# Optimization experiments

Measured on AMD Instinct MI355X. Metric: run time of the kernel, lower is better.

The kernel has to match this reference:

```python
import jax, jax.numpy as jnp
import numpy as np

B, F, D = 4096, 39, 16          # batch, num_field, embedding_size
V = 1000000                     # num_feat (vocab)
H1, H2 = 128, 128               # cin_layer_sizes
INPUT_DIM = F * D               # 624
FC_DIM = H1 // 2 + H2           # 192 (split_half)
DEEP = [400, 400]
BN_EPS = 1e-5


def setup_inputs() -> dict:
    key = jax.random.key(0)
    ks = jax.random.split(key, 16)
    xav = lambda k, shp: jax.random.normal(k, shp, jnp.float32) * np.sqrt(2.0 / (shp[0] + shp[-1]))
    return {
        "feat_index": jax.random.randint(ks[0], (B, F), 0, V),
        "feat_value": jax.random.uniform(ks[1], (B, F), jnp.float32),
        "emb_table": xav(ks[2], (V, D)),
        "linear_w": xav(ks[3], (INPUT_DIM, 1)),
        "linear_b": jnp.zeros((1,), jnp.float32),
        "conv_w1": xav(ks[4], (H1, F, F)),          # (out, h_prev, m) == conv1d 1x1 weight reshaped
        "conv_b1": jnp.zeros((H1,), jnp.float32),
        "conv_w2": xav(ks[5], (H2, H1 // 2, F)),
        "conv_b2": jnp.zeros((H2,), jnp.float32),
        "deep_w1": xav(ks[6], (INPUT_DIM, DEEP[0])),
        "deep_b1": jnp.zeros((DEEP[0],), jnp.float32),
        "bn_g1": jnp.ones((DEEP[0],), jnp.float32),
        "bn_b1": jnp.zeros((DEEP[0],), jnp.float32),
        "deep_w2": xav(ks[7], (DEEP[0], DEEP[1])),
        "deep_b2": jnp.zeros((DEEP[1],), jnp.float32),
        "bn_g2": jnp.ones((DEEP[1],), jnp.float32),
        "bn_b2": jnpp if False else jnp.zeros((DEEP[1],), jnp.float32),
        "out_w": xav(ks[8], (1 + FC_DIM + DEEP[1], 1)),
        "out_b": jnp.zeros((1,), jnp.float32),
    }


def _bn(x, g, b):
    # torch BatchNorm1d in training mode: biased batch variance
    m = x.mean(axis=0)
    v = x.var(axis=0)
    return g * (x - m) * jax.lax.rsqrt(v + BN_EPS) + b


def reference(feat_index, feat_value, emb_table, linear_w, linear_b,
              conv_w1, conv_b1, conv_w2, conv_b2,
              deep_w1, deep_b1, bn_g1, bn_b1,
              deep_w2, deep_b2, bn_g2, bn_b2,
              out_w, out_b):
    e = emb_table[feat_index]                      # [B, F, D]
    flat = e.reshape(e.shape[0], -1)               # [B, F*D]
    linear_part = flat @ linear_w + linear_b       # [B, 1]

    # CIN: fused outer-product + 1x1 conv (x_k[b,o,d] = sum_{h,m} W[o,h,m] x_prev[b,h,d] x0[b,m,d])
    x0 = e
    h1 = jax.nn.relu(jnp.einsum('bhd,bmd,ohm->bod', x0, x0, conv_w1) + conv_b1[None, :, None])
    nxt, hi1 = jnp.split(h1, 2, axis=1)            # split_half
    h2 = jax.nn.relu(jnp.einsum('bhd,bmd,ohm->bod', nxt, x0, conv_w2) + conv_b2[None, :, None])
    res = jnp.concatenate([hi1, h2], axis=1).sum(axis=2)   # [B, FC_DIM]

    # Deep tower (dropout off / deterministic)
    y = jax.nn.relu(_bn(flat @ deep_w1 + deep_b1, bn_g1, bn_b1))
    y = jax.nn.relu(_bn(y @ deep_w2 + deep_b2, bn_g2, bn_b2))

    cat = jnp.concatenate([linear_part, res, y], axis=1)   # [B, 593]
    return cat @ out_w + out_b
```

## Files before the change

kernel.cpp:

```cpp
#include <hip/hip_runtime.h>

#define BATCH   4096
#define NF      39
#define ED      16
#define IN_DIM  624
#define DW      400
#define BN_EPS  1e-5f
#define AK1     640
#define NKS1    20
#define NKS2    13
#define WCOL    416
#define NK1     117
#define NK2     156

typedef __attribute__((ext_vector_type(8))) short short8;
typedef __attribute__((ext_vector_type(16))) float f32x16;
typedef __attribute__((ext_vector_type(4))) float f32x4;
typedef __attribute__((ext_vector_type(2))) float f32x2;
typedef unsigned short u16;

__device__ inline unsigned pack_hi2(float a, float b) {
  return __builtin_amdgcn_perm(__float_as_uint(b), __float_as_uint(a), 0x07060302u);
}
__device__ inline unsigned bf16_rne(float f) {
  unsigned u = __float_as_uint(f);
  u += 0x7fff + ((u >> 16) & 1);
  return u >> 16;
}
__device__ inline float bf2f(u16 v) { return __uint_as_float((unsigned)v << 16); }

#define CIN1_E (NK1 * 2048)
#define CIN2_E (NK2 * 2048)
#define D1_E  (NKS1 * WCOL * 32)
#define D2_E  (NKS2 * WCOL * 32)
#define PREP_E (CIN1_E + CIN2_E + D1_E + D2_E + 1600)
#define PREP_B ((PREP_E + 255) / 256)
#define GATH_B (BATCH / 4)

__global__ __launch_bounds__(256) void k_gp(const int* __restrict__ idx,
    const float* __restrict__ emb, const float* __restrict__ lw,
    const float* __restrict__ lb, const float* __restrict__ w1,
    const float* __restrict__ w2, const float* __restrict__ dw1,
    const float* __restrict__ dw2, u16* __restrict__ flatb,
    float* __restrict__ lp, u16* __restrict__ wp1, u16* __restrict__ wp2,
    u16* __restrict__ wpd1, u16* __restrict__ wpd2, float* __restrict__ gstat) {
  int t = threadIdx.x;
  if (blockIdx.x < GATH_B) {
    int lane = t & 63;
    int b = blockIdx.x * 4 + (t >> 6);
    int sj = (lane < NF) ? idx[b * NF + lane] : 0;
    float acc = 0.f;
#pragma unroll
    for (int i = 0; i < 10; i++) {
      int e = lane + i * 64;
      if (e < IN_DIM) {
        int f = e >> 4;
        int row = __shfl(sj, f);
        float v = emb[(size_t)row * ED + (e & 15)];
        flatb[(size_t)b * AK1 + e] = (u16)bf16_rne(v);
        acc = fmaf(v, lw[e], acc);
      } else {
        flatb[(size_t)b * AK1 + e] = 0;
      }
    }
#pragma unroll
    for (int k = 1; k < 64; k <<= 1) acc += __shfl_xor(acc, k);
    if (lane == 0) lp[b] = acc + lb[0];
  } else {
    int e = (blockIdx.x - GATH_B) * 256 + t;
    if (e < CIN1_E) {
      int k16 = e >> 11, r = e & 2047, col = r >> 4, kk = r & 15;
      int mg = k16 / 3, sg = k16 - mg * 3;
      int h = sg * 16 + kk;
      wp1[e] = (h < NF) ? (u16)bf16_rne(w1[(size_t)col * (NF * NF) + h * NF + mg])
                        : (u16)0;
    } else if (e < CIN1_E + CIN2_E) {
      int e2 = e - CIN1_E;
      int k16 = e2 >> 11, r = e2 & 2047, col = r >> 4, kk = r & 15;
      int k = k16 * 16 + kk, h = k & 63, m = k >> 6;
      wp2[e2] = (u16)bf16_rne(w2[(size_t)col * (64 * NF) + h * NF + m]);
    } else if (e < CIN1_E + CIN2_E + D1_E) {
      int e2 = e - CIN1_E - CIN2_E;
      int ksg = e2 / (WCOL * 32), r = e2 - ksg * (WCOL * 32);
      int col = r >> 5, kk = r & 31;
      int k = ksg * 32 + kk;
      wpd1[e2] = (k < IN_DIM && col < DW) ? (u16)bf16_rne(dw1[(size_t)k * DW + col]) : 0;
    } else if (e < CIN1_E + CIN2_E + D1_E + D2_E) {
      int e2 = e - CIN1_E - CIN2_E - D1_E;
      int ksg = e2 / (WCOL * 32), r = e2 - ksg * (WCOL * 32);
      int col = r >> 5, kk = r & 31;
      int k = ksg * 32 + kk;
      wpd2[e2] = (k < DW && col < DW) ? (u16)bf16_rne(dw2[(size_t)k * DW + col]) : 0;
    } else if (e < PREP_E) {
      gstat[e - CIN1_E - CIN2_E - D1_E - D2_E] = 0.f;
    }
  }
}

__global__ __launch_bounds__(256, 2) void k_cin_f(
    const u16* __restrict__ flatb, const u16* __restrict__ wp1,
    const u16* __restrict__ wp2, const float* __restrict__ bias1,
    const float* __restrict__ bias2, float* __restrict__ res) {
  __shared__ __align__(16) u16 s1b[8 * 16 * 64];
  int t = threadIdx.x;
  int w = t >> 6, lane = t & 63;
  int sgrp = w & 1, oh = w >> 1;
  int col = lane & 31, khalf = lane >> 5;
  int si = (lane >> 4) & 1, d = lane & 15;
  int b0 = blockIdx.x * 8 + sgrp * 4;
  const u16* fb = flatb + (size_t)(b0 + si) * AK1;

  f32x2 sp1[2][3][4];
#pragma unroll
  for (int p = 0; p < 2; p++)
#pragma unroll
    for (int s = 0; s < 3; s++)
#pragma unroll
      for (int w4 = 0; w4 < 4; w4++) {
        int h0 = s * 16 + khalf * 8 + 2 * w4;
        int h1 = h0 + 1;
        float f0 = (h0 < NF) ? bf2f(fb[p * 1280 + h0 * 16 + d]) : 0.f;
        float f1 = (h1 < NF) ? bf2f(fb[p * 1280 + h1 * 16 + d]) : 0.f;
        sp1[p][s][w4] = (f32x2){f0, f1};
      }

  const u16* wb1 = wp1 + (size_t)(oh * 64 + col) * 16 + khalf * 8;
  short8 bfr[3][2];
#pragma unroll
  for (int k16 = 0; k16 < 2; k16++)
#pragma unroll
    for (int nt = 0; nt < 2; nt++)
      bfr[k16][nt] = *(const short8*)(wb1 + (size_t)k16 * 2048 + nt * 512);

  f32x16 acc[2][2];
#pragma unroll
  for (int p = 0; p < 2; p++)
#pragma unroll
    for (int nt = 0; nt < 2; nt++)
#pragma unroll
      for (int r = 0; r < 16; r++) acc[p][nt][r] = 0.f;

  float xv[2] = {bf2f(fb[d]), bf2f(fb[1280 + d])};
  float xvn[2];

#pragma unroll 1
  for (int mg = 0; mg < 13; mg++) {
#pragma unroll
    for (int j = 0; j < 9; j++) {
      int k16 = mg * 9 + j;
      int s = j % 3;
      if (s == 0) {
        int mn = mg * 3 + j / 3 + 1;
        xvn[0] = bf2f(fb[mn * 16 + d]);
        xvn[1] = bf2f(fb[1280 + mn * 16 + d]);
      }
      {
        const u16* wbp = wb1 + (size_t)(k16 + 2) * 2048;
#pragma unroll
        for (int nt = 0; nt < 2; nt++)
          bfr[(s + 2) % 3][nt] = *(const short8*)(wbp + nt * 512);
      }
      __builtin_amdgcn_s_setprio(1);
#pragma unroll
      for (int p = 0; p < 2; p++) {
        union { unsigned u[4]; short8 v; } a;
        f32x2 xv2 = (f32x2){xv[p], xv[p]};
#pragma unroll
        for (int w4 = 0; w4 < 4; w4++) {
          f32x2 pr = sp1[p][s][w4] * xv2;
          a.u[w4] = pack_hi2(pr[0], pr[1]);
        }
#pragma unroll
        for (int nt = 0; nt < 2; nt++)
          acc[p][nt] = __builtin_amdgcn_mfma_f32_32x32x16_bf16(
              a.v, bfr[s][nt], acc[p][nt], 0, 0, 0);
      }
      __builtin_amdgcn_s_setprio(0);
      if (s == 2) { xv[0] = xvn[0]; xv[1] = xvn[1]; }
    }
  }

  if (oh == 0) {
#pragma unroll
    for (int p = 0; p < 2; p++)
#pragma unroll
      for (int nt = 0; nt < 2; nt++) {
        int o = nt * 32 + col;
        float bi = bias1[o];
#pragma unroll
        for (int r = 0; r < 16; r++) {
          int smp = sgrp * 4 + p * 2 + (r >> 3);
          int dd = (r & 3) + 8 * ((r >> 2) & 1) + 4 * khalf;
          float v = fmaxf(acc[p][nt][r] + bi, 0.f);
          int ix = (((smp * 16 + dd) * 64) + o) ^ ((dd & 7) << 3);
          s1b[ix] = (u16)bf16_rne(v);
        }
      }
  } else {
#pragma unroll
    for (int p = 0; p < 2; p++)
#pragma unroll
      for (int nt = 0; nt < 2; nt++) {
        int o = 64 + nt * 32 + col;
        float bi = bias1[o];
        float p0 = 0.f, p1 = 0.f;
#pragma unroll
        for (int r = 0; r < 8; r++)  p0 += fmaxf(acc[p][nt][r] + bi, 0.f);
#pragma unroll
        for (int r = 8; r < 16; r++) p1 += fmaxf(acc[p][nt][r] + bi, 0.f);
        p0 += __shfl_xor(p0, 32);
        p1 += __shfl_xor(p1, 32);
        if (khalf == 0) {
          res[(size_t)(b0 + p * 2) * 192 + (o - 64)] = p0;
          res[(size_t)(b0 + p * 2 + 1) * 192 + (o - 64)] = p1;
        }
      }
  }

  const u16* wb2 = wp2 + (size_t)(oh * 64 + col) * 16 + khalf * 8;
  short8 bq[4][2];
#pragma unroll
  for (int k16 = 0; k16 < 3; k16++)
#pragma unroll
    for (int nt = 0; nt < 2; nt++)
      bq[k16][nt] = *(const short8*)(wb2 + (size_t)k16 * 2048 + nt * 512);

  __syncthreads();

  f32x2 sp2[2][4][4];
#pragma unroll
  for (int p = 0; p < 2; p++) {
    int smp = sgrp * 4 + p * 2 + si;
#pragma unroll
    for (int s = 0; s < 4; s++) {
      int ix = ((smp * 16 + d) * 64 + s * 16 + khalf * 8) ^ ((d & 7) << 3);
      union { short8 v; u16 e[8]; } vv;
      vv.v = *(const short8*)(s1b + ix);
#pragma unroll
      for (int w4 = 0; w4 < 4; w4++)
        sp2[p][s][w4] = (f32x2){bf2f(vv.e[2 * w4]), bf2f(vv.e[2 * w4 + 1])};
    }
  }

#pragma unroll
  for (int p = 0; p < 2; p++)
#pragma unroll
    for (int nt = 0; nt < 2; nt++)
#pragma unroll
      for (int r = 0; r < 16; r++) acc[p][nt][r] = 0.f;

  xv[0] = bf2f(fb[d]);
  xv[1] = bf2f(fb[1280 + d]);

#pragma unroll 1
  for (int mg = 0; mg < 13; mg++) {
#pragma unroll
    for (int j = 0; j < 12; j++) {
      int k16 = mg * 12 + j;
      int s = j & 3;
      if (s == 0) {
        int mn = mg * 3 + (j >> 2) + 1;
        xvn[0] = bf2f(fb[mn * 16 + d]);
        xvn[1] = bf2f(fb[1280 + mn * 16 + d]);
      }
      {
        const u16* wbp = wb2 + (size_t)(k16 + 3) * 2048;
#pragma unroll
        for (int nt = 0; nt < 2; nt++)
          bq[(j + 3) & 3][nt] = *(const short8*)(wbp + nt * 512);
      }
      __builtin_amdgcn_s_setprio(1);
#pragma unroll
      for (int p = 0; p < 2; p++) {
        union { unsigned u[4]; short8 v; } a;
        f32x2 xv2 = (f32x2){xv[p], xv[p]};
#pragma unroll
        for (int w4 = 0; w4 < 4; w4++) {
          f32x2 pr = sp2[p][s][w4] * xv2;
          a.u[w4] = pack_hi2(pr[0], pr[1]);
        }
#pragma unroll
        for (int nt = 0; nt < 2; nt++)
          acc[p][nt] = __builtin_amdgcn_mfma_f32_32x32x16_bf16(
              a.v, bq[s][nt], acc[p][nt], 0, 0, 0);
      }
      __builtin_amdgcn_s_setprio(0);
      if (s == 3) { xv[0] = xvn[0]; xv[1] = xvn[1]; }
    }
  }

#pragma unroll
  for (int p = 0; p < 2; p++)
#pragma unroll
    for (int nt = 0; nt < 2; nt++) {
      int o = oh * 64 + nt * 32 + col;
      float bi = bias2[o];
      float p0 = 0.f, p1 = 0.f;
#pragma unroll
      for (int r = 0; r < 8; r++)  p0 += fmaxf(acc[p][nt][r] + bi, 0.f);
#pragma unroll
      for (int r = 8; r < 16; r++) p1 += fmaxf(acc[p][nt][r] + bi, 0.f);
      p0 += __shfl_xor(p0, 32);
      p1 += __shfl_xor(p1, 32);
      if (khalf == 0) {
        res[(size_t)(b0 + p * 2) * 192 + 64 + o] = p0;
        res[(size_t)(b0 + p * 2 + 1) * 192 + 64 + o] = p1;
      }
    }
}

template <bool BN_A, int NKS, int KREAL, int AK>
__global__ __launch_bounds__(256) void k_gemm_mfma(
    const u16* __restrict__ Abf, const float* __restrict__ Af32,
    const u16* __restrict__ wp, const float* __restrict__ bias,
    const float* __restrict__ gsIn, const float* __restrict__ gs2In,
    const float* __restrict__ bng, const float* __restrict__ bnb,
    float* __restrict__ C, float* __restrict__ gs, float* __restrict__ gs2) {
  __shared__ float lsS[NKS * 32], lsH[NKS * 32];
  __shared__ float lred[64];
  int t = threadIdx.x;
  if (BN_A) {
    for (int c = t; c < NKS * 32; c += 256) {
      float sc = 0.f, sh = 0.f;
      if (c < DW) {
        float m = gsIn[c] * (1.f / BATCH);
        float var = gs2In[c] * (1.f / BATCH) - m * m;
        sc = bng[c] * rsqrtf(var + BN_EPS);
        sh = bnb[c] - m * sc;
      }
      lsS[c] = sc; lsH[c] = sh;
    }
  }
  if (t < 64) lred[t] = 0.f;
  __syncthreads();

  int w = t >> 6, lane = t & 63;
  int nl = lane & 15, q = lane >> 4;
  int row = blockIdx.x * 64 + w * 16 + nl;
  int c0 = blockIdx.y * 32;
  f32x4 acc[2];
  acc[0] = (f32x4){0.f, 0.f, 0.f, 0.f};
  acc[1] = (f32x4){0.f, 0.f, 0.f, 0.f};

  short8 araw[2]; f32x4 fraw0[2], fraw1[2]; short8 braw[2][2];
  auto loadA_raw = [&](int ksg, int buf) {
    int kb = ksg * 32 + q * 8;
    if (!BN_A) {
      araw[buf] = *(const short8*)(Abf + (size_t)row * AK + kb);
    } else {
      if (kb + 8 <= KREAL) {
        fraw0[buf] = *(const f32x4*)(Af32 + (size_t)row * KREAL + kb);
        fraw1[buf] = *(const f32x4*)(Af32 + (size_t)row * KREAL + kb + 4);
      } else {
        fraw0[buf] = (f32x4){0.f,0.f,0.f,0.f};
        fraw1[buf] = (f32x4){0.f,0.f,0.f,0.f};
      }
    }
    const u16* wb = wp + (size_t)ksg * (WCOL * 32) + (size_t)(c0 + nl) * 32 + q * 8;
    braw[buf][0] = *(const short8*)wb;
    braw[buf][1] = *(const short8*)(wb + 16 * 32);
  };
  auto cookA = [&](int ksg, int buf) -> short8 {
    if (!BN_A) return araw[buf];
    int kb = ksg * 32 + q * 8;
    f32x4 s0 = *(const f32x4*)&lsS[kb], h0 = *(const f32x4*)&lsH[kb];
    f32x4 s1 = *(const f32x4*)&lsS[kb + 4], h1 = *(const f32x4*)&lsH[kb + 4];
    union { unsigned u[4]; short8 s; } a;
    float v0 = fmaxf(fmaf(fraw0[buf][0], s0[0], h0[0]), 0.f);
    float v1 = fmaxf(fmaf(fraw0[buf][1], s0[1], h0[1]), 0.f);
    float v2 = fmaxf(fmaf(fraw0[buf][2], s0[2], h0[2]), 0.f);
    float v3 = fmaxf(fmaf(fraw0[buf][3], s0[3], h0[3]), 0.f);
    float v4 = fmaxf(fmaf(fraw1[buf][0], s1[0], h1[0]), 0.f);
    float v5 = fmaxf(fmaf(fraw1[buf][1], s1[1], h1[1]), 0.f);
    float v6 = fmaxf(fmaf(fraw1[buf][2], s1[2], h1[2]), 0.f);
    float v7 = fmaxf(fmaf(fraw1[buf][3], s1[3], h1[3]), 0.f);
    a.u[0] = bf16_rne(v0) | (bf16_rne(v1) << 16);
    a.u[1] = bf16_rne(v2) | (bf16_rne(v3) << 16);
    a.u[2] = bf16_rne(v4) | (bf16_rne(v5) << 16);
    a.u[3] = bf16_rne(v6) | (bf16_rne(v7) << 16);
    return a.s;
  };

  loadA_raw(0, 0);
#pragma unroll 4
  for (int ksg = 0; ksg < NKS; ksg++) {
    int cur = ksg & 1;
    if (ksg + 1 < NKS) loadA_raw(ksg + 1, cur ^ 1);
    short8 afr = cookA(ksg, cur);
    acc[0] = __builtin_amdgcn_mfma_f32_16x16x32_bf16(afr, braw[cur][0], acc[0], 0, 0, 0);
    acc[1] = __builtin_amdgcn_mfma_f32_16x16x32_bf16(afr, braw[cur][1], acc[1], 0, 0, 0);
  }

  int rbase = blockIdx.x * 64 + w * 16 + q * 4;
#pragma unroll
  for (int nt = 0; nt < 2; nt++) {
    int col = c0 + nt * 16 + nl;
    if (col < DW) {
      float bi = bias[col];
      float s = 0.f, s2 = 0.f;
#pragma unroll
      for (int r = 0; r < 4; r++) {
        float v = acc[nt][r] + bi;
        C[(size_t)(rbase + r) * DW + col] = v;
        s += v; s2 = fmaf(v, v, s2);
      }
      s += __shfl_xor(s, 16); s2 += __shfl_xor(s2, 16);
      s += __shfl_xor(s, 32); s2 += __shfl_xor(s2, 32);
      if (q == 0) {
        atomicAdd(&lred[nt * 16 + nl], s);
        atomicAdd(&lred[32 + nt * 16 + nl], s2);
      }
    }
  }
  __syncthreads();
  if (t < 32) {
    int col = c0 + t;
    if (col < DW) atomicAdd(&gs[col], lred[t]);
  } else if (t < 64) {
    int col = c0 + t - 32;
    if (col < DW) atomicAdd(&gs2[col], lred[t]);
  }
}

__global__ __launch_bounds__(256) void k_final(const float* __restrict__ lp,
    const float* __restrict__ res, const float* __restrict__ y2,
    const float* __restrict__ gB, const float* __restrict__ gB2,
    const float* __restrict__ g2, const float* __restrict__ bb2,
    const float* __restrict__ ow, const float* __restrict__ ob,
    float* __restrict__ out) {
  __shared__ float lsS[DW], lsH[DW];
  int t = threadIdx.x;
  for (int c = t; c < DW; c += 256) {
    float m = gB[c] * (1.f / BATCH);
    float var = gB2[c] * (1.f / BATCH) - m * m;
    float sc = g2[c] * rsqrtf(var + BN_EPS);
    lsS[c] = sc;
    lsH[c] = bb2[c] - m * sc;
  }
  __syncthreads();
  int lane = t & 63, w = t >> 6;
  int b = blockIdx.x * 4 + w;
  float acc = 0.f;
  for (int j = lane; j < 593; j += 64) {
    float v;
    if (j == 0)       v = lp[b];
    else if (j < 193) v = res[(size_t)b * 192 + (j - 1)];
    else {
      int c = j - 193;
      v = fmaxf(fmaf(y2[(size_t)b * DW + c], lsS[c], lsH[c]), 0.f);
    }
    acc = fmaf(v, ow[j], acc);
  }
#pragma unroll
  for (int k = 1; k < 64; k <<= 1) acc += __shfl_xor(acc, k);
  if (lane == 0) out[b] = acc + ob[0];
}

extern "C" void kernel_launch(void* const* d_in, const int* in_sizes, int n_in,
                              void* d_out, int out_size, void* d_ws, size_t ws_size,
                              hipStream_t stream) {
  const int*   feat_index = (const int*)d_in[0];
  const float* emb = (const float*)d_in[2];
  const float* lw  = (const float*)d_in[3];
  const float* lb  = (const float*)d_in[4];
  const float* w1  = (const float*)d_in[5];
  const float* b1  = (const float*)d_in[6];
  const float* w2  = (const float*)d_in[7];
  const float* b2  = (const float*)d_in[8];
  const float* dw1 = (const float*)d_in[9];
  const float* db1 = (const float*)d_in[10];
  const float* g1  = (const float*)d_in[11];
  const float* bb1 = (const float*)d_in[12];
  const float* dw2 = (const float*)d_in[13];
  const float* db2 = (const float*)d_in[14];
  const float* g2  = (const float*)d_in[15];
  const float* bb2 = (const float*)d_in[16];
  const float* ow  = (const float*)d_in[17];
  const float* ob  = (const float*)d_in[18];

  float* ws   = (float*)d_ws;
  u16*  flatb = (u16*)ws;
  float* y1   = ws + 1310720;
  float* res  = ws + 2949120;
  float* lp   = ws + 3735552;
  float* gA   = ws + 3741248;
  float* gA2  = gA + 400;
  float* gB   = gA2 + 400;
  float* gB2  = gB + 400;
  float* y2   = ws + 3742848;
  u16*  wp1   = (u16*)(ws + 5381248);
  u16*  wp2   = (u16*)(ws + 5501056);
  u16*  wpd1  = (u16*)(ws + 5660800);
  u16*  wpd2  = (u16*)(ws + 5793920);
  float* out  = (float*)d_out;

  k_gp<<<GATH_B + PREP_B, 256, 0, stream>>>(feat_index, emb, lw, lb, w1, w2,
      dw1, dw2, flatb, lp, wp1, wp2, wpd1, wpd2, gA);
  k_cin_f<<<512, 256, 0, stream>>>(flatb, wp1, wp2, b1, b2, res);
  k_gemm_mfma<false, NKS1, IN_DIM, AK1><<<dim3(BATCH / 64, 13), 256, 0, stream>>>(
      flatb, nullptr, wpd1, db1, nullptr, nullptr, nullptr, nullptr, y1, gA, gA2);
  k_gemm_mfma<true, NKS2, DW, 0><<<dim3(BATCH / 64, 13), 256, 0, stream>>>(
      nullptr, y1, wpd2, db2, gA, gA2, g1, bb1, y2, gB, gB2);
  k_final<<<BATCH / 4, 256, 0, stream>>>(lp, res, y2, gB, gB2, g2, bb2, ow, ob, out);
}
```

Measured before the change: 246.9 us.

## Split CIN kernel work so each wave owns one 32-column tile over 4 samples

```diff
diff --git a/kernel.cpp b/kernel.cpp
--- a/kernel.cpp
+++ b/kernel.cpp
@@ -97,17 +97,16 @@
   }
 }
 
-__global__ __launch_bounds__(256, 2) void k_cin_f(
+__global__ __launch_bounds__(256, 4) void k_cin_f(
     const u16* __restrict__ flatb, const u16* __restrict__ wp1,
     const u16* __restrict__ wp2, const float* __restrict__ bias1,
     const float* __restrict__ bias2, float* __restrict__ res) {
-  __shared__ __align__(16) u16 s1b[8 * 16 * 64];
+  __shared__ __align__(16) u16 s1b[4 * 16 * 64];
   int t = threadIdx.x;
-  int w = t >> 6, lane = t & 63;
-  int sgrp = w & 1, oh = w >> 1;
+  int ow = t >> 6, lane = t & 63;
   int col = lane & 31, khalf = lane >> 5;
   int si = (lane >> 4) & 1, d = lane & 15;
-  int b0 = blockIdx.x * 8 + sgrp * 4;
+  int b0 = blockIdx.x * 4;
   const u16* fb = flatb + (size_t)(b0 + si) * AK1;
 
   f32x2 sp1[2][3][4];
@@ -124,21 +123,16 @@
         sp1[p][s][w4] = (f32x2){f0, f1};
       }
 
-  const u16* wb1 = wp1 + (size_t)(oh * 64 + col) * 16 + khalf * 8;
-  short8 bfr[3][2];
-#pragma unroll
-  for (int k16 = 0; k16 < 2; k16++)
-#pragma unroll
-    for (int nt = 0; nt < 2; nt++)
-      bfr[k16][nt] = *(const short8*)(wb1 + (size_t)k16 * 2048 + nt * 512);
-
-  f32x16 acc[2][2];
+  const u16* wb1 = wp1 + (size_t)(ow * 32 + col) * 16 + khalf * 8;
+  short8 bfr[3];
+  bfr[0] = *(const short8*)(wb1);
+  bfr[1] = *(const short8*)(wb1 + 2048);
+
+  f32x16 acc[2];
 #pragma unroll
   for (int p = 0; p < 2; p++)
 #pragma unroll
-    for (int nt = 0; nt < 2; nt++)
-#pragma unroll
-      for (int r = 0; r < 16; r++) acc[p][nt][r] = 0.f;
+    for (int r = 0; r < 16; r++) acc[p][r] = 0.f;
 
   float xv[2] = {bf2f(fb[d]), bf2f(fb[1280 + d])};
   float xvn[2];
@@ -154,12 +148,7 @@
         xvn[0] = bf2f(fb[mn * 16 + d]);
         xvn[1] = bf2f(fb[1280 + mn * 16 + d]);
       }
-      {
-        const u16* wbp = wb1 + (size_t)(k16 + 2) * 2048;
-#pragma unroll
-        for (int nt = 0; nt < 2; nt++)
-          bfr[(s + 2) % 3][nt] = *(const short8*)(wbp + nt * 512);
-      }
+      bfr[(s + 2) % 3] = *(const short8*)(wb1 + (size_t)(k16 + 2) * 2048);
       __builtin_amdgcn_s_setprio(1);
 #pragma unroll
       for (int p = 0; p < 2; p++) {
@@ -170,67 +159,59 @@
           f32x2 pr = sp1[p][s][w4] * xv2;
           a.u[w4] = pack_hi2(pr[0], pr[1]);
         }
-#pragma unroll
-        for (int nt = 0; nt < 2; nt++)
-          acc[p][nt] = __builtin_amdgcn_mfma_f32_32x32x16_bf16(
-              a.v, bfr[s][nt], acc[p][nt], 0, 0, 0);
+        acc[p] = __builtin_amdgcn_mfma_f32_32x32x16_bf16(
+            a.v, bfr[s], acc[p], 0, 0, 0);
       }
       __builtin_amdgcn_s_setprio(0);
       if (s == 2) { xv[0] = xvn[0]; xv[1] = xvn[1]; }
     }
   }
 
-  if (oh == 0) {
-#pragma unroll
-    for (int p = 0; p < 2; p++)
-#pragma unroll
-      for (int nt = 0; nt < 2; nt++) {
-        int o = nt * 32 + col;
-        float bi = bias1[o];
-#pragma unroll
-        for (int r = 0; r < 16; r++) {
-          int smp = sgrp * 4 + p * 2 + (r >> 3);
-          int dd = (r & 3) + 8 * ((r >> 2) & 1) + 4 * khalf;
-          float v = fmaxf(acc[p][nt][r] + bi, 0.f);
-          int ix = (((smp * 16 + dd) * 64) + o) ^ ((dd & 7) << 3);
-          s1b[ix] = (u16)bf16_rne(v);
-        }
-      }
+  if (ow < 2) {
+#pragma unroll
+    for (int p = 0; p < 2; p++) {
+      int o = ow * 32 + col;
+      float bi = bias1[o];
+#pragma unroll
+      for (int r = 0; r < 16; r++) {
+        int smp = p * 2 + (r >> 3);
+        int dd = (r & 3) + 8 * ((r >> 2) & 1) + 4 * khalf;
+        float v = fmaxf(acc[p][r] + bi, 0.f);
+        int ix = (((smp * 16 + dd) * 64) + o) ^ ((dd & 7) << 3);
+        s1b[ix] = (u16)bf16_rne(v);
+      }
+    }
   } else {
 #pragma unroll
-    for (int p = 0; p < 2; p++)
-#pragma unroll
-      for (int nt = 0; nt < 2; nt++) {
-        int o = 64 + nt * 32 + col;
-        float bi = bias1[o];
-        float p0 = 0.f, p1 = 0.f;
-#pragma unroll
-        for (int r = 0; r < 8; r++)  p0 += fmaxf(acc[p][nt][r] + bi, 0.f);
-#pragma unroll
-        for (int r = 8; r < 16; r++) p1 += fmaxf(acc[p][nt][r] + bi, 0.f);
-        p0 += __shfl_xor(p0, 32);
-        p1 += __shfl_xor(p1, 32);
-        if (khalf == 0) {
-          res[(size_t)(b0 + p * 2) * 192 + (o - 64)] = p0;
-          res[(size_t)(b0 + p * 2 + 1) * 192 + (o - 64)] = p1;
-        }
-      }
-  }
-
-  const u16* wb2 = wp2 + (size_t)(oh * 64 + col) * 16 + khalf * 8;
-  short8 bq[4][2];
-#pragma unroll
-  for (int k16 = 0; k16 < 3; k16++)
-#pragma unroll
-    for (int nt = 0; nt < 2; nt++)
-      bq[k16][nt] = *(const short8*)(wb2 + (size_t)k16 * 2048 + nt * 512);
+    for (int p = 0; p < 2; p++) {
+      int o = ow * 32 + col;
+      float bi = bias1[o];
+      float p0 = 0.f, p1 = 0.f;
+#pragma unroll
+      for (int r = 0; r < 8; r++)  p0 += fmaxf(acc[p][r] + bi, 0.f);
+#pragma unroll
+      for (int r = 8; r < 16; r++) p1 += fmaxf(acc[p][r] + bi, 0.f);
+      p0 += __shfl_xor(p0, 32);
+      p1 += __shfl_xor(p1, 32);
+      if (khalf == 0) {
+        res[(size_t)(b0 + p * 2) * 192 + (o - 64)] = p0;
+        res[(size_t)(b0 + p * 2 + 1) * 192 + (o - 64)] = p1;
+      }
+    }
+  }
+
+  const u16* wb2 = wp2 + (size_t)(ow * 32 + col) * 16 + khalf * 8;
+  short8 bq[4];
+  bq[0] = *(const short8*)(wb2);
+  bq[1] = *(const short8*)(wb2 + 2048);
+  bq[2] = *(const short8*)(wb2 + 4096);
 
   __syncthreads();
 
   f32x2 sp2[2][4][4];
 #pragma unroll
   for (int p = 0; p < 2; p++) {
-    int smp = sgrp * 4 + p * 2 + si;
+    int smp = p * 2 + si;
 #pragma unroll
     for (int s = 0; s < 4; s++) {
       int ix = ((smp * 16 + d) * 64 + s * 16 + khalf * 8) ^ ((d & 7) << 3);
@@ -245,9 +226,7 @@
 #pragma unroll
   for (int p = 0; p < 2; p++)
 #pragma unroll
-    for (int nt = 0; nt < 2; nt++)
-#pragma unroll
-      for (int r = 0; r < 16; r++) acc[p][nt][r] = 0.f;
+    for (int r = 0; r < 16; r++) acc[p][r] = 0.f;
 
   xv[0] = bf2f(fb[d]);
   xv[1] = bf2f(fb[1280 + d]);
@@ -263,12 +242,7 @@
         xvn[0] = bf2f(fb[mn * 16 + d]);
         xvn[1] = bf2f(fb[1280 + mn * 16 + d]);
       }
-      {
-        const u16* wbp = wb2 + (size_t)(k16 + 3) * 2048;
-#pragma unroll
-        for (int nt = 0; nt < 2; nt++)
-          bq[(j + 3) & 3][nt] = *(const short8*)(wbp + nt * 512);
-      }
+      bq[(j + 3) & 3] = *(const short8*)(wb2 + (size_t)(k16 + 3) * 2048);
       __builtin_amdgcn_s_setprio(1);
 #pragma unroll
       for (int p = 0; p < 2; p++) {
@@ -279,10 +253,8 @@
           f32x2 pr = sp2[p][s][w4] * xv2;
           a.u[w4] = pack_hi2(pr[0], pr[1]);
         }
-#pragma unroll
-        for (int nt = 0; nt < 2; nt++)
-          acc[p][nt] = __builtin_amdgcn_mfma_f32_32x32x16_bf16(
-              a.v, bq[s][nt], acc[p][nt], 0, 0, 0);
+        acc[p] = __builtin_amdgcn_mfma_f32_32x32x16_bf16(
+            a.v, bq[s], acc[p], 0, 0, 0);
       }
       __builtin_amdgcn_s_setprio(0);
       if (s == 3) { xv[0] = xvn[0]; xv[1] = xvn[1]; }
@@ -290,23 +262,21 @@
   }
 
 #pragma unroll
-  for (int p = 0; p < 2; p++)
-#pragma unroll
-    for (int nt = 0; nt < 2; nt++) {
-      int o = oh * 64 + nt * 32 + col;
-      float bi = bias2[o];
-      float p0 = 0.f, p1 = 0.f;
-#pragma unroll
-      for (int r = 0; r < 8; r++)  p0 += fmaxf(acc[p][nt][r] + bi, 0.f);
-#pragma unroll
-      for (int r = 8; r < 16; r++) p1 += fmaxf(acc[p][nt][r] + bi, 0.f);
-      p0 += __shfl_xor(p0, 32);
-      p1 += __shfl_xor(p1, 32);
-      if (khalf == 0) {
-        res[(size_t)(b0 + p * 2) * 192 + 64 + o] = p0;
-        res[(size_t)(b0 + p * 2 + 1) * 192 + 64 + o] = p1;
-      }
-    }
+  for (int p = 0; p < 2; p++) {
+    int o = ow * 32 + col;
+    float bi = bias2[o];
+    float p0 = 0.f, p1 = 0.f;
+#pragma unroll
+    for (int r = 0; r < 8; r++)  p0 += fmaxf(acc[p][r] + bi, 0.f);
+#pragma unroll
+    for (int r = 8; r < 16; r++) p1 += fmaxf(acc[p][r] + bi, 0.f);
+    p0 += __shfl_xor(p0, 32);
+    p1 += __shfl_xor(p1, 32);
+    if (khalf == 0) {
+      res[(size_t)(b0 + p * 2) * 192 + 64 + o] = p0;
+      res[(size_t)(b0 + p * 2 + 1) * 192 + 64 + o] = p1;
+    }
+  }
 }
 
 template <bool BN_A, int NKS, int KREAL, int AK>
@@ -496,7 +466,7 @@
 
   k_gp<<<GATH_B + PREP_B, 256, 0, stream>>>(feat_index, emb, lw, lb, w1, w2,
       dw1, dw2, flatb, lp, wp1, wp2, wpd1, wpd2, gA);
-  k_cin_f<<<512, 256, 0, stream>>>(flatb, wp1, wp2, b1, b2, res);
+  k_cin_f<<<1024, 256, 0, stream>>>(flatb, wp1, wp2, b1, b2, res);
   k_gemm_mfma<false, NKS1, IN_DIM, AK1><<<dim3(BATCH / 64, 13), 256, 0, stream>>>(
       flatb, nullptr, wpd1, db1, nullptr, nullptr, nullptr, nullptr, y1, gA, gA2);
   k_gemm_mfma<true, NKS2, DW, 0><<<dim3(BATCH / 64, 13), 256, 0, stream>>>(
```

Result: slower. 298.1 us (+20.7%).
